# Kernel tuning notes

Hardware: AMD Instinct MI355X
Metric: run time of the kernel (lower is better)

Reference implementation:

```python
import jax, jax.numpy as jnp
import numpy as np

DIM = 128
HEADS = 4
DIM_HEAD = 32
N_EMBD = HEADS * DIM_HEAD  # 128
SCALE = DIM_HEAD ** -0.5


def conv2d(x, w, b):
    # NCHW conv, 3x3, stride 1, SAME padding (= padding=1 in torch)
    out = jax.lax.conv_general_dilated(
        x, w, window_strides=(1, 1), padding='SAME',
        dimension_numbers=('NCHW', 'OIHW', 'NCHW'))
    return out + b[None, :, None, None]


def conv_block(x, w1, b1, w2, b2):
    # Conv -> ReLU -> Conv (the to_q/to_k/to_v pattern)
    return conv2d(jax.nn.relu(conv2d(x, w1, b1)), w2, b2)


def setup_inputs() -> dict:
    key = jax.random.key(0)
    ks = jax.random.split(key, 20)
    B, C, S = 4, DIM, 32
    H, W = 128, 512
    wscale = 0.05

    def cw(k, cout, cin):
        return jax.random.normal(k, (cout, cin, 3, 3), jnp.float32) * wscale

    inp = {
        'x': jax.random.normal(ks[0], (B, C, S, S), jnp.float32),
        'y': jax.random.normal(ks[1], (B, C, H, W), jnp.float32),
        'u': jax.random.randint(ks[2], (B, S, S), 0, W),
        'q_w1': cw(ks[3], N_EMBD, DIM), 'q_b1': jnp.zeros((N_EMBD,), jnp.float32),
        'q_w2': cw(ks[4], N_EMBD, N_EMBD), 'q_b2': jnp.zeros((N_EMBD,), jnp.float32),
        'k_w1': cw(ks[5], N_EMBD, DIM), 'k_b1': jnp.zeros((N_EMBD,), jnp.float32),
        'k_w2': cw(ks[6], N_EMBD, N_EMBD), 'k_b2': jnp.zeros((N_EMBD,), jnp.float32),
        'v_w1': cw(ks[7], N_EMBD, DIM), 'v_b1': jnp.zeros((N_EMBD,), jnp.float32),
        'v_w2': cw(ks[8], N_EMBD, N_EMBD), 'v_b2': jnp.zeros((N_EMBD,), jnp.float32),
        'proj_w': cw(ks[9], DIM, N_EMBD), 'proj_b': jnp.zeros((DIM,), jnp.float32),
    }
    return inp


def reference(x, y, u, q_w1, q_b1, q_w2, q_b2, k_w1, k_b1, k_w2, k_b2,
              v_w1, v_b1, v_w2, v_b2, proj_w, proj_b):
    B, C, S, _ = x.shape
    _, _, H, W = y.shape
    SS = S * S

    # Q from the (B,C,S,S) query grid -> (B, S^2, n_embd)
    q = conv_block(x, q_w1, q_b1, q_w2, q_b2).reshape(B, N_EMBD, SS).transpose(0, 2, 1)

    # K, V from the (B,C,H,W) map
    k = conv_block(y, k_w1, k_b1, k_w2, k_b2)  # (B, E, H, W)
    v = conv_block(y, v_w1, v_b1, v_w2, v_b2)

    # Gather columns of K/V along W per query index u (clamped)
    uc = jnp.clip(u, 0, W - 1).astype(jnp.int32).reshape(B, 1, 1, SS)
    ks = jnp.take_along_axis(k, uc, axis=3).transpose(0, 3, 2, 1)  # (B, SS, H, E)
    vs = jnp.take_along_axis(v, uc, axis=3).transpose(0, 3, 2, 1)  # (B, SS, H, E)

    # Per-query attention over the H axis
    dot = SCALE * jnp.einsum('bqe,bqhe->bqh', q, ks)  # (B, SS, H)
    attn = jax.nn.softmax(dot, axis=-1)
    a = jnp.einsum('bqh,bqhe->bqe', attn, vs)  # (B, SS, E)

    a = a.transpose(0, 2, 1).reshape(B, N_EMBD, S, S)
    z = jax.nn.relu(conv2d(a, proj_w, proj_b))  # (B, DIM, S, S)
    return z
```

## Files before the change

### kernel.cpp

```cpp
#include <hip/hip_runtime.h>
#include <stdint.h>

typedef __attribute__((ext_vector_type(16))) float f32x16;
typedef __attribute__((ext_vector_type(8))) short s16x8;

#define WAITVM(n) asm volatile("s_waitcnt vmcnt(" #n ")" ::: "memory")
#define WAITLGKM0 asm volatile("s_waitcnt lgkmcnt(0)" ::: "memory")

__device__ inline short bf16b(float f) {
  uint32_t x = __float_as_uint(f);
  return (short)((x + 0x7fffu + ((x >> 16) & 1u)) >> 16);
}
__device__ inline float bfu(uint16_t u) { return __uint_as_float(((uint32_t)u) << 16); }

__device__ inline void gll16(const void* g, void* l) {
  __builtin_amdgcn_global_load_lds((const __attribute__((address_space(1))) void*)g,
                                   (__attribute__((address_space(3))) void*)l, 16, 0, 0);
}

__global__ __launch_bounds__(256) void packw_k(
    const float* w0, const float* w1, const float* w2, const float* w3,
    const float* w4, const float* w5, const float* w6, s16x8* dst) {
  const float* srcs[7] = {w0, w1, w2, w3, w4, w5, w6};
  const int widx = blockIdx.y;
  const float* src = srcs[widx];
  const int gid = blockIdx.x * 256 + threadIdx.x;
  const int lane = gid & 63, frag = gid >> 6;
  const int nblk = frag & 3, ks = (frag >> 2) & 1, chunk = (frag >> 3) & 3, tap = frag >> 5;
  const int co = nblk * 32 + (lane & 31);
  const int cib = chunk * 32 + ks * 16 + (lane >> 5) * 8;
  s16x8 v;
#pragma unroll
  for (int j = 0; j < 8; ++j)
    v[j] = bf16b(src[((size_t)co * 128 + cib + j) * 9 + tap]);
  dst[(size_t)widx * 18432 + (size_t)frag * 64 + lane] = v;
}

template <int TW>
__global__ __launch_bounds__(256) void nchw2nhwc_k(
    const float* __restrict__ in, uint16_t* __restrict__ out, int H, int W) {
  __shared__ float tile[128][TW + 1];
  const int b = blockIdx.z, h = blockIdx.y, w0 = blockIdx.x * TW;
  for (int idx = threadIdx.x; idx < 128 * TW; idx += 256) {
    int c = idx / TW, w = idx - c * TW;
    tile[c][w] = in[(((size_t)b * 128 + c) * H + h) * W + w0 + w];
  }
  __syncthreads();
  for (int idx = threadIdx.x; idx < TW * 16; idx += 256) {
    int w = idx >> 4, cg = idx & 15;
    s16x8 v;
#pragma unroll
    for (int j = 0; j < 8; ++j) v[j] = bf16b(tile[cg * 8 + j][w]);
    *reinterpret_cast<s16x8*>(out + ((((size_t)b * H + h) * W + w0 + w) << 7) + cg * 8) = v;
  }
}

template <int OMODE, bool RELU, typename Tout>
__global__ __launch_bounds__(256, 2) void convmf8_k(
    const uint16_t* __restrict__ in, const s16x8* __restrict__ wpk,
    const float* __restrict__ bias, Tout* __restrict__ out,
    const uint16_t* __restrict__ zp, int H, int W) {
  constexpr int CP = 34, RP = 6, RPCP = RP * CP;
  constexpr int SLOTS = 4 * RPCP;
  constexpr int SPT = 4;
  __shared__ s16x8 lds[2][SPT * 256];
  const int b = blockIdx.z, r0 = blockIdx.y * 4, c0 = blockIdx.x * 32;
  const int tid = threadIdx.x, lane = tid & 63, wn = tid >> 6;
  const int wbase = tid & 192;

  const uint16_t* gsrc[SPT];
#pragma unroll
  for (int i = 0; i < SPT; ++i) {
    const int s = tid + i * 256;
    const int kq = s / RPCP;
    const int rem = s - kq * RPCP;
    const int r = rem / CP, c = rem - r * CP;
    const int gr = r0 + r - 1, gc = c0 + c - 1;
    const bool ok = (s < SLOTS) && gr >= 0 && gr < H && gc >= 0 && gc < W;
    gsrc[i] = ok ? (in + (((size_t)b * H + gr) * W + gc) * 128 + kq * 8) : zp;
  }

  const s16x8* __restrict__ wbl = wpk + wn * 64 + lane;
  s16x8 wf[2][9];
#pragma unroll
  for (int ks = 0; ks < 2; ++ks)
#pragma unroll
    for (int t = 0; t < 9; ++t) wf[ks][t] = wbl[(t * 8 + ks) * 256];

#pragma unroll
  for (int i = 0; i < SPT; ++i) gll16(gsrc[i], &lds[0][wbase + i * 256]);

  f32x16 acc[4];
#pragma unroll
  for (int i = 0; i < 4; ++i)
#pragma unroll
    for (int r = 0; r < 16; ++r) acc[i][r] = 0.f;

  const int abase = (lane >> 5) * RPCP + (lane & 31);
  WAITVM(0);
  __builtin_amdgcn_s_barrier();
  __builtin_amdgcn_sched_barrier(0);

#pragma unroll
  for (int chunk = 0; chunk < 4; ++chunk) {
    const int cb = chunk & 1;
    const s16x8* __restrict__ Lb = &lds[cb][abase];
#pragma unroll
    for (int p = 0; p < 3; ++p) {
      const int kx = p;
      s16x8 ar[2][6];
#pragma unroll
      for (int ks = 0; ks < 2; ++ks)
#pragma unroll
        for (int r = 0; r < 6; ++r) ar[ks][r] = Lb[ks * 2 * RPCP + r * CP + kx];
      if (chunk < 3 && p < 2) {
        gll16(gsrc[2 * p] + (chunk + 1) * 32, &lds[cb ^ 1][wbase + (2 * p) * 256]);
        gll16(gsrc[2 * p + 1] + (chunk + 1) * 32, &lds[cb ^ 1][wbase + (2 * p + 1) * 256]);
      }
      __builtin_amdgcn_sched_barrier(0);
      WAITLGKM0;
      __builtin_amdgcn_sched_barrier(0);
      __builtin_amdgcn_s_setprio(1);
#pragma unroll
      for (int ks = 0; ks < 2; ++ks) {
#pragma unroll
        for (int ky = 0; ky < 3; ++ky) {
#pragma unroll
          for (int mf = 0; mf < 4; ++mf)
            acc[mf] = __builtin_amdgcn_mfma_f32_32x32x16_bf16(ar[ks][mf + ky], wf[ks][ky * 3 + kx],
                                                              acc[mf], 0, 0, 0);
        }
      }
      __builtin_amdgcn_s_setprio(0);
      if (chunk < 3) {
#pragma unroll
        for (int ks = 0; ks < 2; ++ks)
#pragma unroll
          for (int ky = 0; ky < 3; ++ky) {
            const int tap = ky * 3 + kx;
            wf[ks][tap] = wbl[((tap * 4 + chunk + 1) * 2 + ks) * 256];
          }
      }
      __builtin_amdgcn_sched_barrier(0);
    }
    if (chunk < 3) {
      WAITVM(12);
      __builtin_amdgcn_s_barrier();
      __builtin_amdgcn_sched_barrier(0);
    }
  }

  const int co = wn * 32 + (lane & 31);
  const float bv = bias[co];
#pragma unroll
  for (int mf = 0; mf < 4; ++mf) {
    const int gr = r0 + mf;
#pragma unroll
    for (int reg = 0; reg < 16; ++reg) {
      const int gc = c0 + (reg & 3) + 8 * (reg >> 2) + 4 * (lane >> 5);
      float v = acc[mf][reg] + bv;
      if (RELU) v = fmaxf(v, 0.f);
      size_t idx;
      if (OMODE == 0)      idx = (((size_t)b * H + gr) * W + gc) * 128 + co;
      else if (OMODE == 1) idx = (((size_t)b * W + gc) * H + gr) * 128 + co;
      else                 idx = (((size_t)b * 128 + co) * H + gr) * W + gc;
      if constexpr (sizeof(Tout) == 2) ((uint16_t*)out)[idx] = (uint16_t)bf16b(v);
      else out[idx] = v;
    }
  }
}

__global__ __launch_bounds__(128) void attn_dot_k(
    const float* __restrict__ qg, const uint16_t* __restrict__ Kg,
    const int* __restrict__ u, float* __restrict__ pout) {
  const int bs = blockIdx.x;
  const int b = bs >> 10;
  const int tid = threadIdx.x;
  __shared__ float sq[128];
  __shared__ float wred[2][2];
  sq[tid] = qg[(size_t)bs * 128 + tid];
  int w = u[bs]; w = w < 0 ? 0 : (w > 511 ? 511 : w);
  __syncthreads();
  const s16x8* kp = reinterpret_cast<const s16x8*>(
      Kg + (((size_t)b * 512 + w) * 128 + tid) * 128);
  float acc = 0.f;
#pragma unroll
  for (int i = 0; i < 16; ++i) {
    s16x8 v = kp[i];
#pragma unroll
    for (int j = 0; j < 8; ++j)
      acc = fmaf(sq[i * 8 + j], bfu((uint16_t)v[j]), acc);
  }
  const float d = acc * 0.17677669529663687f;
  float m = d;
#pragma unroll
  for (int o = 1; o < 64; o <<= 1) m = fmaxf(m, __shfl_xor(m, o));
  if ((tid & 63) == 0) wred[0][tid >> 6] = m;
  __syncthreads();
  m = fmaxf(wred[0][0], wred[0][1]);
  const float e = expf(d - m);
  float s = e;
#pragma unroll
  for (int o = 1; o < 64; o <<= 1) s += __shfl_xor(s, o);
  if ((tid & 63) == 0) wred[1][tid >> 6] = s;
  __syncthreads();
  s = wred[1][0] + wred[1][1];
  pout[(size_t)bs * 128 + tid] = e / s;
}

__global__ __launch_bounds__(128) void attn_pv_k(
    const float* __restrict__ pin, const uint16_t* __restrict__ Vg,
    const int* __restrict__ u, uint16_t* __restrict__ aout) {
  const int bs = blockIdx.x;
  const int b = bs >> 10;
  const int tid = threadIdx.x;
  const int eo = tid & 15, hg = tid >> 4;
  __shared__ float sp[128];
  __shared__ float red[8][128];
  sp[tid] = pin[(size_t)bs * 128 + tid];
  int w = u[bs]; w = w < 0 ? 0 : (w > 511 ? 511 : w);
  __syncthreads();
  const s16x8* vp = reinterpret_cast<const s16x8*>(
      Vg + ((size_t)b * 512 + w) * 16384) + eo;
  float a8[8];
#pragma unroll
  for (int j = 0; j < 8; ++j) a8[j] = 0.f;
#pragma unroll
  for (int hh = 0; hh < 16; ++hh) {
    const int h = hg * 16 + hh;
    s16x8 v = vp[h * 16];
    const float p = sp[h];
#pragma unroll
    for (int j = 0; j < 8; ++j) a8[j] = fmaf(p, bfu((uint16_t)v[j]), a8[j]);
  }
#pragma unroll
  for (int j = 0; j < 8; ++j) red[hg][eo * 8 + j] = a8[j];
  __syncthreads();
  float r = 0.f;
#pragma unroll
  for (int g = 0; g < 8; ++g) r += red[g][tid];
  aout[(size_t)bs * 128 + tid] = (uint16_t)bf16b(r);
}

extern "C" void kernel_launch(void* const* d_in, const int* in_sizes, int n_in,
                              void* d_out, int out_size, void* d_ws, size_t ws_size,
                              hipStream_t stream) {
  const float* x      = (const float*)d_in[0];
  const float* y      = (const float*)d_in[1];
  const int*   u      = (const int*)d_in[2];
  const float* q_w1   = (const float*)d_in[3];
  const float* q_b1   = (const float*)d_in[4];
  const float* q_w2   = (const float*)d_in[5];
  const float* q_b2   = (const float*)d_in[6];
  const float* k_w1   = (const float*)d_in[7];
  const float* k_b1   = (const float*)d_in[8];
  const float* k_w2   = (const float*)d_in[9];
  const float* k_b2   = (const float*)d_in[10];
  const float* v_w1   = (const float*)d_in[11];
  const float* v_b1   = (const float*)d_in[12];
  const float* v_w2   = (const float*)d_in[13];
  const float* v_b2   = (const float*)d_in[14];
  const float* proj_w = (const float*)d_in[15];
  const float* proj_b = (const float*)d_in[16];
  float* out = (float*)d_out;

  char* ws = (char*)d_ws;
  const size_t MB = 1 << 20;
  const size_t BIG = 64 * MB;
  const bool tierB = ws_size >= 203 * MB;
  uint16_t* A  = (uint16_t*)ws;
  uint16_t* Bb = (uint16_t*)(ws + BIG);
  uint16_t* KV = tierB ? (uint16_t*)(ws + 2 * BIG) : A;
  char* sm = ws + (tierB ? 3 : 2) * BIG;
  float*    qg  = (float*)sm;
  float*    pb  = (float*)(sm + 2 * MB);
  uint16_t* xbf = (uint16_t*)(sm + 4 * MB);
  uint16_t* t1  = (uint16_t*)(sm + 5 * MB);
  uint16_t* ab  = (uint16_t*)(sm + 6 * MB);
  s16x8*    wpk = (s16x8*)(sm + 7 * MB);
  uint16_t* zp  = (uint16_t*)(sm + 10 * MB);

  hipMemsetAsync(zp, 0, 1024, stream);
  packw_k<<<dim3(72, 7), 256, 0, stream>>>(q_w1, q_w2, k_w1, k_w2, v_w1, v_w2, proj_w, wpk);
  nchw2nhwc_k<32><<<dim3(1, 32, 4), 256, 0, stream>>>(x, xbf, 32, 32);
  nchw2nhwc_k<64><<<dim3(8, 128, 4), 256, 0, stream>>>(y, A, 128, 512);
  convmf8_k<0, true,  uint16_t><<<dim3(1, 8, 4), 256, 0, stream>>>(xbf, wpk + 0 * 18432, q_b1, t1, zp, 32, 32);
  convmf8_k<0, false, float   ><<<dim3(1, 8, 4), 256, 0, stream>>>(t1,  wpk + 1 * 18432, q_b2, qg, zp, 32, 32);
  convmf8_k<0, true,  uint16_t><<<dim3(16, 32, 4), 256, 0, stream>>>(A,  wpk + 2 * 18432, k_b1, Bb, zp, 128, 512);
  convmf8_k<1, false, uint16_t><<<dim3(16, 32, 4), 256, 0, stream>>>(Bb, wpk + 3 * 18432, k_b2, KV, zp, 128, 512);
  attn_dot_k<<<dim3(4096), 128, 0, stream>>>(qg, KV, u, pb);
  if (!tierB) nchw2nhwc_k<64><<<dim3(8, 128, 4), 256, 0, stream>>>(y, A, 128, 512);
  convmf8_k<0, true,  uint16_t><<<dim3(16, 32, 4), 256, 0, stream>>>(A,  wpk + 4 * 18432, v_b1, Bb, zp, 128, 512);
  convmf8_k<1, false, uint16_t><<<dim3(16, 32, 4), 256, 0, stream>>>(Bb, wpk + 5 * 18432, v_b2, KV, zp, 128, 512);
  attn_pv_k<<<dim3(4096), 128, 0, stream>>>(pb, KV, u, ab);
  convmf8_k<3, true, float><<<dim3(1, 8, 4), 256, 0, stream>>>(ab, wpk + 6 * 18432, proj_b, out, zp, 32, 32);
}
```

Baseline: 446.7 us.

## Halve weight register footprint in conv kernel to raise occupancy to three blocks

The MFMA conv kernel now holds only one k-slice of weights (9 fragments instead of 18) and splits each chunk into six phases instead of three. The next weights are prefetched one phase ahead, and the launch bound is raised to allow three blocks per CU. This cuts VGPR pressure so more waves can hide latency. In exchange it adds an extra workgroup barrier per phase and changes the vmcnt wait threshold, which adds synchronisation overhead and leaves less slack for weight prefetch.

New measurement: 430.8 us. -3.6%, faster.

```diff
diff --git a/kernel.cpp b/kernel.cpp
--- a/kernel.cpp
+++ b/kernel.cpp
@@ -56,7 +56,7 @@
 }
 
 template <int OMODE, bool RELU, typename Tout>
-__global__ __launch_bounds__(256, 2) void convmf8_k(
+__global__ __launch_bounds__(256, 3) void convmf7_k(
     const uint16_t* __restrict__ in, const s16x8* __restrict__ wpk,
     const float* __restrict__ bias, Tout* __restrict__ out,
     const uint16_t* __restrict__ zp, int H, int W) {
@@ -81,11 +81,9 @@
   }
 
   const s16x8* __restrict__ wbl = wpk + wn * 64 + lane;
-  s16x8 wf[2][9];
-#pragma unroll
-  for (int ks = 0; ks < 2; ++ks)
-#pragma unroll
-    for (int t = 0; t < 9; ++t) wf[ks][t] = wbl[(t * 8 + ks) * 256];
+  s16x8 wf[9];
+#pragma unroll
+  for (int t = 0; t < 9; ++t) wf[t] = wbl[t * 2048];
 
 #pragma unroll
   for (int i = 0; i < SPT; ++i) gll16(gsrc[i], &lds[0][wbase + i * 256]);
@@ -106,47 +104,38 @@
     const int cb = chunk & 1;
     const s16x8* __restrict__ Lb = &lds[cb][abase];
 #pragma unroll
-    for (int p = 0; p < 3; ++p) {
-      const int kx = p;
-      s16x8 ar[2][6];
-#pragma unroll
-      for (int ks = 0; ks < 2; ++ks)
-#pragma unroll
-        for (int r = 0; r < 6; ++r) ar[ks][r] = Lb[ks * 2 * RPCP + r * CP + kx];
-      if (chunk < 3 && p < 2) {
-        gll16(gsrc[2 * p] + (chunk + 1) * 32, &lds[cb ^ 1][wbase + (2 * p) * 256]);
-        gll16(gsrc[2 * p + 1] + (chunk + 1) * 32, &lds[cb ^ 1][wbase + (2 * p + 1) * 256]);
-      }
+    for (int p = 0; p < 6; ++p) {
+      const int ks = p / 3, kx = p - ks * 3;
+      s16x8 ar[6];
+#pragma unroll
+      for (int r = 0; r < 6; ++r) ar[r] = Lb[ks * 2 * RPCP + r * CP + kx];
+      if (chunk < 3 && p < SPT)
+        gll16(gsrc[p] + (chunk + 1) * 32, &lds[cb ^ 1][wbase + p * 256]);
       __builtin_amdgcn_sched_barrier(0);
+      __builtin_amdgcn_s_barrier();
       WAITLGKM0;
       __builtin_amdgcn_sched_barrier(0);
       __builtin_amdgcn_s_setprio(1);
 #pragma unroll
-      for (int ks = 0; ks < 2; ++ks) {
+      for (int ky = 0; ky < 3; ++ky) {
+#pragma unroll
+        for (int mf = 0; mf < 4; ++mf)
+          acc[mf] = __builtin_amdgcn_mfma_f32_32x32x16_bf16(ar[mf + ky], wf[ky * 3 + kx],
+                                                            acc[mf], 0, 0, 0);
+      }
+      __builtin_amdgcn_s_setprio(0);
+      if (!(chunk == 3 && ks == 1)) {
+        const int nc = (ks == 0) ? chunk : chunk + 1;
+        const int nks = (ks == 0) ? 1 : 0;
 #pragma unroll
         for (int ky = 0; ky < 3; ++ky) {
-#pragma unroll
-          for (int mf = 0; mf < 4; ++mf)
-            acc[mf] = __builtin_amdgcn_mfma_f32_32x32x16_bf16(ar[ks][mf + ky], wf[ks][ky * 3 + kx],
-                                                              acc[mf], 0, 0, 0);
+          const int tap = ky * 3 + kx;
+          wf[tap] = wbl[((tap * 4 + nc) * 2 + nks) * 256];
         }
       }
-      __builtin_amdgcn_s_setprio(0);
-      if (chunk < 3) {
-#pragma unroll
-        for (int ks = 0; ks < 2; ++ks)
-#pragma unroll
-          for (int ky = 0; ky < 3; ++ky) {
-            const int tap = ky * 3 + kx;
-            wf[ks][tap] = wbl[((tap * 4 + chunk + 1) * 2 + ks) * 256];
-          }
-      }
       __builtin_amdgcn_sched_barrier(0);
-    }
-    if (chunk < 3) {
-      WAITVM(12);
+      if (p == 5 && chunk < 3) WAITVM(9);
       __builtin_amdgcn_s_barrier();
-      __builtin_amdgcn_sched_barrier(0);
     }
   }
 
@@ -284,14 +273,14 @@
   packw_k<<<dim3(72, 7), 256, 0, stream>>>(q_w1, q_w2, k_w1, k_w2, v_w1, v_w2, proj_w, wpk);
   nchw2nhwc_k<32><<<dim3(1, 32, 4), 256, 0, stream>>>(x, xbf, 32, 32);
   nchw2nhwc_k<64><<<dim3(8, 128, 4), 256, 0, stream>>>(y, A, 128, 512);
-  convmf8_k<0, true,  uint16_t><<<dim3(1, 8, 4), 256, 0, stream>>>(xbf, wpk + 0 * 18432, q_b1, t1, zp, 32, 32);
-  convmf8_k<0, false, float   ><<<dim3(1, 8, 4), 256, 0, stream>>>(t1,  wpk + 1 * 18432, q_b2, qg, zp, 32, 32);
-  convmf8_k<0, true,  uint16_t><<<dim3(16, 32, 4), 256, 0, stream>>>(A,  wpk + 2 * 18432, k_b1, Bb, zp, 128, 512);
-  convmf8_k<1, false, uint16_t><<<dim3(16, 32, 4), 256, 0, stream>>>(Bb, wpk + 3 * 18432, k_b2, KV, zp, 128, 512);
+  convmf7_k<0, true,  uint16_t><<<dim3(1, 8, 4), 256, 0, stream>>>(xbf, wpk + 0 * 18432, q_b1, t1, zp, 32, 32);
+  convmf7_k<0, false, float   ><<<dim3(1, 8, 4), 256, 0, stream>>>(t1,  wpk + 1 * 18432, q_b2, qg, zp, 32, 32);
+  convmf7_k<0, true,  uint16_t><<<dim3(16, 32, 4), 256, 0, stream>>>(A,  wpk + 2 * 18432, k_b1, Bb, zp, 128, 512);
+  convmf7_k<1, false, uint16_t><<<dim3(16, 32, 4), 256, 0, stream>>>(Bb, wpk + 3 * 18432, k_b2, KV, zp, 128, 512);
   attn_dot_k<<<dim3(4096), 128, 0, stream>>>(qg, KV, u, pb);
   if (!tierB) nchw2nhwc_k<64><<<dim3(8, 128, 4), 256, 0, stream>>>(y, A, 128, 512);
-  convmf8_k<0, true,  uint16_t><<<dim3(16, 32, 4), 256, 0, stream>>>(A,  wpk + 4 * 18432, v_b1, Bb, zp, 128, 512);
-  convmf8_k<1, false, uint16_t><<<dim3(16, 32, 4), 256, 0, stream>>>(Bb, wpk + 5 * 18432, v_b2, KV, zp, 128, 512);
+  convmf7_k<0, true,  uint16_t><<<dim3(16, 32, 4), 256, 0, stream>>>(A,  wpk + 4 * 18432, v_b1, Bb, zp, 128, 512);
+  convmf7_k<1, false, uint16_t><<<dim3(16, 32, 4), 256, 0, stream>>>(Bb, wpk + 5 * 18432, v_b2, KV, zp, 128, 512);
   attn_pv_k<<<dim3(4096), 128, 0, stream>>>(pb, KV, u, ab);
-  convmf8_k<3, true, float><<<dim3(1, 8, 4), 256, 0, stream>>>(ab, wpk + 6 * 18432, proj_b, out, zp, 32, 32);
-}
+  convmf7_k<3, true, float><<<dim3(1, 8, 4), 256, 0, stream>>>(ab, wpk + 6 * 18432, proj_b, out, zp, 32, 32);
+}
```
